# Kernel optimization log

Measured on AMD Instinct MI355X. Metric: run time of the kernel, lower is better.

Reference implementation:

```python
import jax, jax.numpy as jnp
import numpy as np

B, N, C, H = 1, 4096, 512, 8
S = 64  # sqrt(N), static


def setup_inputs() -> dict:
    key = jax.random.key(0)
    ks = jax.random.split(key, 4)
    d = C // H
    return {
        "x": jax.random.normal(ks[0], (B, N, C), dtype=jnp.float32),
        "num_heads": H,
        "bias": jnp.zeros((1,), dtype=jnp.float32),  # unused in original forward
        "scale": jnp.asarray(d ** -0.5, dtype=jnp.float32),
        "Wqkv": jax.random.normal(ks[1], (3 * C, C), dtype=jnp.float32) * (C ** -0.5),
        "bqkv": jnp.zeros((3 * C,), dtype=jnp.float32),
        "Wproj": jax.random.normal(ks[2], (C, C), dtype=jnp.float32) * (C ** -0.5),
        "bproj": jnp.zeros((C,), dtype=jnp.float32),
    }


def reference(x, num_heads, bias, scale, Wqkv, bqkv, Wproj, bproj):
    b, n, c = x.shape
    d = c // num_heads
    # fused QKV projection: [b, n, 3c] -> [3, b, h, n, d]
    qkv = (x @ Wqkv.T + bqkv).reshape(b, n, 3, num_heads, d).transpose(2, 0, 3, 1, 4)
    q, k, v = qkv[0] * scale, qkv[1], qkv[2]
    attn = jax.nn.softmax(jnp.einsum("bhnd,bhmd->bhnm", q, k), axis=-1)
    out = jnp.einsum("bhnm,bhmd->bhnd", attn, v)
    out = out.transpose(0, 2, 1, 3).reshape(b, n, c)
    out = out @ Wproj.T + bproj
    return out.reshape(b, S, S, c)
```

## Files before the change

kernel.cpp:

```cpp
#include <hip/hip_runtime.h>
#include <stdint.h>

#define NTOK 4096
#define CDIM 512
#define HEADS 8
#define DHEAD 64
#define PHEAD (NTOK * DHEAD)

typedef __bf16 bf16x8 __attribute__((ext_vector_type(8)));
typedef float f32x4 __attribute__((ext_vector_type(4)));

__device__ __forceinline__ unsigned short bfbits(float f) {
    return __builtin_bit_cast(unsigned short, (__bf16)f);
}

__device__ __forceinline__ f32x4 mfma32(bf16x8 a, bf16x8 b, f32x4 c) {
    return __builtin_amdgcn_mfma_f32_16x16x32_bf16(a, b, c, 0, 0, 0);
}

__device__ __forceinline__ void async16(unsigned short* lds, const unsigned short* g) {
    __builtin_amdgcn_global_load_lds(
        (const __attribute__((address_space(1))) unsigned int*)g,
        (__attribute__((address_space(3))) unsigned int*)lds, 16, 0, 0);
}

__device__ __forceinline__ void stage8(unsigned short* dst, const float* src) {
    const float4 v0 = *(const float4*)src;
    const float4 v1 = *(const float4*)(src + 4);
    ushort4 o0, o1;
    o0.x = bfbits(v0.x); o0.y = bfbits(v0.y); o0.z = bfbits(v0.z); o0.w = bfbits(v0.w);
    o1.x = bfbits(v1.x); o1.y = bfbits(v1.y); o1.z = bfbits(v1.z); o1.w = bfbits(v1.w);
    *(ushort4*)dst = o0;
    *(ushort4*)(dst + 4) = o1;
}

__global__ __launch_bounds__(256) void gemm_qkv(
    const float* __restrict__ A,
    const float* __restrict__ Bm,
    const float* __restrict__ bias,
    const float* __restrict__ scale_p,
    unsigned short* __restrict__ qkv_out)
{
    const int K = CDIM, Nn = 3 * CDIM; (void)Nn;
    __shared__ __align__(16) unsigned short smem[128 * 136];
    unsigned short* lA = smem;
    unsigned short* lB = smem + 4096;

    const int tid = threadIdx.x;
    const int mBase = blockIdx.y * 128, nBase = blockIdx.x * 128;
    const int lane = tid & 63;
    const int w = __builtin_amdgcn_readfirstlane(tid >> 6);
    const int l16 = lane & 15, quad = lane >> 4;
    const int wr = (w >> 1) * 64, wc = (w & 1) * 64;
    const int srow = tid >> 2, scol = (tid & 3) * 8;

    f32x4 acc[4][4] = {};

    for (int kt = 0; kt < K; kt += 32) {
        __syncthreads();
#pragma unroll
        for (int p = 0; p < 2; ++p) {
            const int r = p * 64 + srow;
            stage8(&lA[r * 32 + scol], &A[(size_t)(mBase + r) * K + kt + scol]);
            stage8(&lB[r * 32 + scol], &Bm[(size_t)(nBase + r) * K + kt + scol]);
        }
        __syncthreads();

        bf16x8 af[4], bfr[4];
#pragma unroll
        for (int i = 0; i < 4; ++i)
            af[i] = *(const bf16x8*)&lA[(wr + i * 16 + l16) * 32 + quad * 8];
#pragma unroll
        for (int j = 0; j < 4; ++j)
            bfr[j] = *(const bf16x8*)&lB[(wc + j * 16 + l16) * 32 + quad * 8];
#pragma unroll
        for (int i = 0; i < 4; ++i)
#pragma unroll
            for (int j = 0; j < 4; ++j)
                acc[i][j] = mfma32(af[i], bfr[j], acc[i][j]);
    }

    const int three = nBase >> 9;
    const float scl = scale_p[0] * 1.44269504f;
    const float mul = (three == 0) ? scl : 1.0f;

    __syncthreads();
#pragma unroll
    for (int i = 0; i < 4; ++i)
#pragma unroll
        for (int j = 0; j < 4; ++j)
#pragma unroll
            for (int r = 0; r < 4; ++r) {
                const int rl = wr + i * 16 + quad * 4 + r;
                const int cl = wc + j * 16 + l16;
                const float v = (acc[i][j][r] + bias[nBase + cl]) * mul;
                smem[rl * 136 + cl] = bfbits(v);
            }
    __syncthreads();

    const size_t base3 = (size_t)three * (PHEAD * HEADS);
    if (three < 2) {
#pragma unroll
        for (int pass = 0; pass < 8; ++pass) {
            const int idx = pass * 256 + tid;
            const int rl16 = idx & 15, qc = (idx >> 4) & 7;
            const int hsel = (idx >> 7) & 1, t16l = (idx >> 8) & 7;
            const uint4 d = *(const uint4*)&smem[(t16l * 16 + rl16) * 136 + hsel * 64 + qc * 8];
            const int hh = ((nBase >> 6) + hsel) & 7;
            const int t16 = (mBase >> 4) + t16l;
            const size_t dst = base3 + (size_t)hh * PHEAD +
                (size_t)(((t16 * 2 + (qc >> 2)) * 64 + (qc & 3) * 16 + rl16) * 8);
            *(uint4*)&qkv_out[dst] = d;
        }
    } else {
#pragma unroll
        for (int pass = 0; pass < 8; ++pass) {
            const int idx = pass * 256 + tid;
            const int l16t = idx & 15, quadt = (idx >> 4) & 3;
            const int dt = (idx >> 6) & 3, k32l = (idx >> 8) & 3, hsel = (idx >> 10) & 1;
            const int col = hsel * 64 + dt * 16 + l16t;
            unsigned short o8[8];
#pragma unroll
            for (int e = 0; e < 4; ++e) {
                o8[e]     = smem[(k32l * 32 + quadt * 4 + e) * 136 + col];
                o8[e + 4] = smem[(k32l * 32 + 16 + quadt * 4 + e) * 136 + col];
            }
            const int hh = ((nBase >> 6) + hsel) & 7;
            const int k32 = (mBase >> 5) + k32l;
            const size_t dst = base3 + (size_t)hh * PHEAD +
                (size_t)(((k32 * 4 + dt) * 64 + quadt * 16 + l16t) * 8);
            *(uint4*)&qkv_out[dst] = *(uint4*)o8;
        }
    }
}

__global__ __launch_bounds__(256) void gemm_proj(
    const unsigned short* __restrict__ A,
    const float* __restrict__ Bm,
    const float* __restrict__ bias,
    float* __restrict__ c_out)
{
    const int K = CDIM, Nn = CDIM;
    __shared__ __align__(16) unsigned short smem[128 * 64];
    unsigned short* lA = smem;
    unsigned short* lB = smem + 4096;

    const int tid = threadIdx.x;
    const int mBase = blockIdx.y * 128, nBase = blockIdx.x * 128;
    const int lane = tid & 63;
    const int w = __builtin_amdgcn_readfirstlane(tid >> 6);
    const int l16 = lane & 15, quad = lane >> 4;
    const int wr = (w >> 1) * 64, wc = (w & 1) * 64;
    const int arow = lane >> 2, acol = (lane & 3) * 8;
    const int srow = tid >> 2, scol = (tid & 3) * 8;

    f32x4 acc[4][4] = {};

    for (int kt = 0; kt < K; kt += 32) {
        __syncthreads();
#pragma unroll
        for (int i = 0; i < 2; ++i) {
            const int r0 = (w * 2 + i) * 16;
            async16(&lA[r0 * 32], &A[(size_t)(mBase + r0 + arow) * K + kt + acol]);
        }
#pragma unroll
        for (int p = 0; p < 2; ++p) {
            const int r = p * 64 + srow;
            stage8(&lB[r * 32 + scol], &Bm[(size_t)(nBase + r) * K + kt + scol]);
        }
        __syncthreads();

        bf16x8 af[4], bfr[4];
#pragma unroll
        for (int i = 0; i < 4; ++i)
            af[i] = *(const bf16x8*)&lA[(wr + i * 16 + l16) * 32 + quad * 8];
#pragma unroll
        for (int j = 0; j < 4; ++j)
            bfr[j] = *(const bf16x8*)&lB[(wc + j * 16 + l16) * 32 + quad * 8];
#pragma unroll
        for (int i = 0; i < 4; ++i)
#pragma unroll
            for (int j = 0; j < 4; ++j)
                acc[i][j] = mfma32(af[i], bfr[j], acc[i][j]);
    }

#pragma unroll
    for (int i = 0; i < 4; ++i)
#pragma unroll
        for (int j = 0; j < 4; ++j)
#pragma unroll
            for (int r = 0; r < 4; ++r) {
                const int grow = mBase + wr + i * 16 + quad * 4 + r;
                const int gcol = nBase + wc + j * 16 + l16;
                c_out[(size_t)grow * Nn + gcol] = acc[i][j][r] + bias[gcol];
            }
}

__global__ __launch_bounds__(256, 4) void flash6_k(
    const unsigned short* __restrict__ qf,
    const unsigned short* __restrict__ kf,
    const unsigned short* __restrict__ vf,
    unsigned short* __restrict__ attn_out)
{
    __shared__ float ldsO[4][32][68];
    __shared__ float sml[4][32];

    const int tid = threadIdx.x;
    const int lane = tid & 63;
    const int w = __builtin_amdgcn_readfirstlane(tid >> 6);
    const int l16 = lane & 15, quad = lane >> 4;
    const int h = blockIdx.x, qb = blockIdx.y;

    const unsigned short* qh = qf + (size_t)h * PHEAD;
    const unsigned short* kb = kf + (size_t)h * PHEAD + w * 65536;
    const unsigned short* vb = vf + (size_t)h * PHEAD + w * 65536;

    bf16x8 qfr[2][2];
#pragma unroll
    for (int qt = 0; qt < 2; ++qt)
#pragma unroll
        for (int ks = 0; ks < 2; ++ks)
            qfr[qt][ks] = *(const bf16x8*)&qh[((qb * 2 + qt) * 2 + ks) * 512 + lane * 8];

    bf16x8 ones;
#pragma unroll
    for (int j = 0; j < 8; ++j) ones[j] = (__bf16)1.0f;

    f32x4 oacc[4][2] = {};
    f32x4 lacc[2] = {};

    bf16x8 kA[4], kB[4];
#pragma unroll
    for (int i = 0; i < 4; ++i)
        kA[i] = *(const bf16x8*)&kb[i * 512 + lane * 8];

    auto body = [&](int g, bf16x8* kuse, bf16x8* kload) {
#pragma unroll
        for (int i = 0; i < 4; ++i)
            kload[i] = *(const bf16x8*)&kb[(g + 1) * 2048 + i * 512 + lane * 8];
        bf16x8 vc[4];
#pragma unroll
        for (int i = 0; i < 4; ++i)
            vc[i] = *(const bf16x8*)&vb[g * 2048 + i * 512 + lane * 8];

        f32x4 s[2][2];
#pragma unroll
        for (int kt = 0; kt < 2; ++kt)
#pragma unroll
            for (int qt = 0; qt < 2; ++qt) {
                f32x4 a = {};
                a = mfma32(kuse[kt * 2 + 0], qfr[qt][0], a);
                a = mfma32(kuse[kt * 2 + 1], qfr[qt][1], a);
                s[kt][qt] = a;
            }

        bf16x8 pf[2];
#pragma unroll
        for (int qt = 0; qt < 2; ++qt) {
            bf16x8 pb;
#pragma unroll
            for (int kt = 0; kt < 2; ++kt)
#pragma unroll
                for (int r = 0; r < 4; ++r)
                    pb[kt * 4 + r] = (__bf16)__builtin_amdgcn_exp2f(s[kt][qt][r]);
            pf[qt] = pb;
            lacc[qt] = mfma32(ones, pb, lacc[qt]);
        }
#pragma unroll
        for (int dt = 0; dt < 4; ++dt)
#pragma unroll
            for (int qt = 0; qt < 2; ++qt)
                oacc[dt][qt] = mfma32(vc[dt], pf[qt], oacc[dt][qt]);
    };

    for (int it = 0; it < 16; ++it) {
        body(it * 2 + 0, kA, kB);
        body(it * 2 + 1, kB, kA);
    }

    if (quad == 0) {
#pragma unroll
        for (int qt = 0; qt < 2; ++qt) sml[w][qt * 16 + l16] = lacc[qt][0];
    }
    __syncthreads();
#pragma unroll
    for (int qt = 0; qt < 2; ++qt) {
        const int q = qt * 16 + l16;
#pragma unroll
        for (int dt = 0; dt < 4; ++dt)
            *(f32x4*)&ldsO[w][q][dt * 16 + quad * 4] = oacc[dt][qt];
    }
    __syncthreads();
    {
        const int q = tid >> 3, dseg = (tid & 7) * 8;
        const float L = sml[0][q] + sml[1][q] + sml[2][q] + sml[3][q];
        const float inv = 1.f / L;
        unsigned short o8[8];
#pragma unroll
        for (int i = 0; i < 8; ++i) {
            const float v = ldsO[0][q][dseg + i] + ldsO[1][q][dseg + i] +
                            ldsO[2][q][dseg + i] + ldsO[3][q][dseg + i];
            o8[i] = bfbits(v * inv);
        }
        *(uint4*)&attn_out[(size_t)(qb * 32 + q) * CDIM + h * DHEAD + dseg] = *(uint4*)o8;
    }
}

extern "C" void kernel_launch(void* const* d_in, const int* in_sizes, int n_in,
                              void* d_out, int out_size, void* d_ws, size_t ws_size,
                              hipStream_t stream) {
    const float* x       = (const float*)d_in[0];
    const float* scale_p = (const float*)d_in[3];
    const float* Wqkv    = (const float*)d_in[4];
    const float* bqkv    = (const float*)d_in[5];
    const float* Wproj   = (const float*)d_in[6];
    const float* bproj   = (const float*)d_in[7];
    float* out = (float*)d_out;

    char* ws = (char*)d_ws;
    const size_t OFF_QKV  = 0;
    const size_t OFF_ATTN = 12582912;
    const size_t NEEDED   = OFF_ATTN + 4194304;
    if (ws_size < NEEDED) return;

    unsigned short* qkvb  = (unsigned short*)(ws + OFF_QKV);
    unsigned short* attnb = (unsigned short*)(ws + OFF_ATTN);

    gemm_qkv<<<dim3(12, 32), 256, 0, stream>>>(x, Wqkv, bqkv, scale_p, qkvb);

    const unsigned short* qfr = qkvb;
    const unsigned short* kfr = qkvb + (size_t)PHEAD * HEADS;
    const unsigned short* vfr = qkvb + (size_t)2 * PHEAD * HEADS;
    flash6_k<<<dim3(8, 128), 256, 0, stream>>>(qfr, kfr, vfr, attnb);

    gemm_proj<<<dim3(4, 32), 256, 0, stream>>>(attnb, Wproj, bproj, out);
}
```

Before: 152.1 us.

## Split attention over key halves with atomic accumulation and deferred normalization

```diff
diff --git a/kernel.cpp b/kernel.cpp
--- a/kernel.cpp
+++ b/kernel.cpp
@@ -16,12 +16,6 @@
 
 __device__ __forceinline__ f32x4 mfma32(bf16x8 a, bf16x8 b, f32x4 c) {
     return __builtin_amdgcn_mfma_f32_16x16x32_bf16(a, b, c, 0, 0, 0);
-}
-
-__device__ __forceinline__ void async16(unsigned short* lds, const unsigned short* g) {
-    __builtin_amdgcn_global_load_lds(
-        (const __attribute__((address_space(1))) unsigned int*)g,
-        (__attribute__((address_space(3))) unsigned int*)lds, 16, 0, 0);
 }
 
 __device__ __forceinline__ void stage8(unsigned short* dst, const float* src) {
@@ -41,7 +35,7 @@
     const float* __restrict__ scale_p,
     unsigned short* __restrict__ qkv_out)
 {
-    const int K = CDIM, Nn = 3 * CDIM; (void)Nn;
+    const int K = CDIM;
     __shared__ __align__(16) unsigned short smem[128 * 136];
     unsigned short* lA = smem;
     unsigned short* lB = smem + 4096;
@@ -134,8 +128,126 @@
     }
 }
 
+__global__ __launch_bounds__(256, 2) void flash7_k(
+    const unsigned short* __restrict__ qf,
+    const unsigned short* __restrict__ kf,
+    const unsigned short* __restrict__ vf,
+    float* __restrict__ attn_acc,
+    float* __restrict__ l_acc)
+{
+    __shared__ float ldsO[2][64][68];
+
+    const int tid = threadIdx.x;
+    const int lane = tid & 63;
+    const int w = __builtin_amdgcn_readfirstlane(tid >> 6);
+    const int l16 = lane & 15, quad = lane >> 4;
+    const int h = blockIdx.x, qb = blockIdx.y, ks = blockIdx.z;
+
+    const unsigned short* qh = qf + (size_t)h * PHEAD;
+    const unsigned short* kb = kf + (size_t)h * PHEAD + ks * 131072 + w * 32768;
+    const unsigned short* vb = vf + (size_t)h * PHEAD + ks * 131072 + w * 32768;
+
+    bf16x8 qfr[4][2];
+#pragma unroll
+    for (int qt = 0; qt < 4; ++qt)
+#pragma unroll
+        for (int d2 = 0; d2 < 2; ++d2)
+            qfr[qt][d2] = *(const bf16x8*)&qh[((qb * 4 + qt) * 2 + d2) * 512 + lane * 8];
+
+    bf16x8 ones;
+#pragma unroll
+    for (int j = 0; j < 8; ++j) ones[j] = (__bf16)1.0f;
+
+    f32x4 oacc[4][4] = {};
+    f32x4 lacc[4] = {};
+
+    bf16x8 kA[4], kB[4];
+#pragma unroll
+    for (int i = 0; i < 4; ++i)
+        kA[i] = *(const bf16x8*)&kb[i * 512 + lane * 8];
+
+    auto body = [&](int g, bf16x8* kuse, bf16x8* kload) {
+#pragma unroll
+        for (int i = 0; i < 4; ++i)
+            kload[i] = *(const bf16x8*)&kb[(g + 1) * 2048 + i * 512 + lane * 8];
+        bf16x8 vc[4];
+#pragma unroll
+        for (int i = 0; i < 4; ++i)
+            vc[i] = *(const bf16x8*)&vb[g * 2048 + i * 512 + lane * 8];
+
+        f32x4 s[2][4];
+#pragma unroll
+        for (int kt = 0; kt < 2; ++kt)
+#pragma unroll
+            for (int qt = 0; qt < 4; ++qt) {
+                f32x4 a = {};
+                a = mfma32(kuse[kt * 2 + 0], qfr[qt][0], a);
+                a = mfma32(kuse[kt * 2 + 1], qfr[qt][1], a);
+                s[kt][qt] = a;
+            }
+
+        bf16x8 pf[4];
+#pragma unroll
+        for (int qt = 0; qt < 4; ++qt) {
+            bf16x8 pb;
+#pragma unroll
+            for (int kt = 0; kt < 2; ++kt)
+#pragma unroll
+                for (int r = 0; r < 4; ++r)
+                    pb[kt * 4 + r] = (__bf16)__builtin_amdgcn_exp2f(s[kt][qt][r]);
+            pf[qt] = pb;
+            lacc[qt] = mfma32(ones, pb, lacc[qt]);
+        }
+#pragma unroll
+        for (int dt = 0; dt < 4; ++dt)
+#pragma unroll
+            for (int qt = 0; qt < 4; ++qt)
+                oacc[dt][qt] = mfma32(vc[dt], pf[qt], oacc[dt][qt]);
+    };
+
+    for (int it = 0; it < 8; ++it) {
+        body(it * 2 + 0, kA, kB);
+        body(it * 2 + 1, kB, kA);
+    }
+
+    if (w == 0 || w == 2) {
+        const int b = w >> 1;
+#pragma unroll
+        for (int qt = 0; qt < 4; ++qt)
+#pragma unroll
+            for (int dt = 0; dt < 4; ++dt)
+                *(f32x4*)&ldsO[b][qt * 16 + l16][dt * 16 + quad * 4] = oacc[dt][qt];
+    }
+    if (quad == 0) {
+#pragma unroll
+        for (int qt = 0; qt < 4; ++qt)
+            atomicAdd(&l_acc[h * NTOK + qb * 64 + qt * 16 + l16], lacc[qt][0]);
+    }
+    __syncthreads();
+    if (w == 1 || w == 3) {
+        const int b = w >> 1;
+#pragma unroll
+        for (int qt = 0; qt < 4; ++qt)
+#pragma unroll
+            for (int dt = 0; dt < 4; ++dt) {
+                float* p = &ldsO[b][qt * 16 + l16][dt * 16 + quad * 4];
+                const f32x4 prev = *(const f32x4*)p;
+                *(f32x4*)p = prev + oacc[dt][qt];
+            }
+    }
+    __syncthreads();
+    {
+        const int q = tid >> 2, db = (tid & 3) * 16;
+        float* dst = &attn_acc[(size_t)(qb * 64 + q) * CDIM + h * DHEAD + db];
+#pragma unroll
+        for (int j = 0; j < 16; ++j)
+            atomicAdd(dst + j, ldsO[0][q][db + j] + ldsO[1][q][db + j]);
+    }
+}
+
 __global__ __launch_bounds__(256) void gemm_proj(
-    const unsigned short* __restrict__ A,
+    const float* __restrict__ A,
+    const float* __restrict__ l_acc,
     const float* __restrict__ Bm,
     const float* __restrict__ bias,
     float* __restrict__ c_out)
@@ -151,21 +263,26 @@
     const int w = __builtin_amdgcn_readfirstlane(tid >> 6);
     const int l16 = lane & 15, quad = lane >> 4;
     const int wr = (w >> 1) * 64, wc = (w & 1) * 64;
-    const int arow = lane >> 2, acol = (lane & 3) * 8;
     const int srow = tid >> 2, scol = (tid & 3) * 8;
 
     f32x4 acc[4][4] = {};
 
     for (int kt = 0; kt < K; kt += 32) {
+        const int head = kt >> 6;
         __syncthreads();
-#pragma unroll
-        for (int i = 0; i < 2; ++i) {
-            const int r0 = (w * 2 + i) * 16;
-            async16(&lA[r0 * 32], &A[(size_t)(mBase + r0 + arow) * K + kt + acol]);
-        }
 #pragma unroll
         for (int p = 0; p < 2; ++p) {
             const int r = p * 64 + srow;
+            const float invl = __builtin_amdgcn_rcpf(l_acc[head * NTOK + mBase + r]);
+            const float4 v0 = *(const float4*)&A[(size_t)(mBase + r) * K + kt + scol];
+            const float4 v1 = *(const float4*)&A[(size_t)(mBase + r) * K + kt + scol + 4];
+            ushort4 o0, o1;
+            o0.x = bfbits(v0.x * invl); o0.y = bfbits(v0.y * invl);
+            o0.z = bfbits(v0.z * invl); o0.w = bfbits(v0.w * invl);
+            o1.x = bfbits(v1.x * invl); o1.y = bfbits(v1.y * invl);
+            o1.z = bfbits(v1.z * invl); o1.w = bfbits(v1.w * invl);
+            *(ushort4*)&lA[r * 32 + scol] = o0;
+            *(ushort4*)&lA[r * 32 + scol + 4] = o1;
             stage8(&lB[r * 32 + scol], &Bm[(size_t)(nBase + r) * K + kt + scol]);
         }
         __syncthreads();
@@ -194,116 +311,6 @@
                 const int gcol = nBase + wc + j * 16 + l16;
                 c_out[(size_t)grow * Nn + gcol] = acc[i][j][r] + bias[gcol];
             }
-}
-
-__global__ __launch_bounds__(256, 4) void flash6_k(
-    const unsigned short* __restrict__ qf,
-    const unsigned short* __restrict__ kf,
-    const unsigned short* __restrict__ vf,
-    unsigned short* __restrict__ attn_out)
-{
-    __shared__ float ldsO[4][32][68];
-    __shared__ float sml[4][32];
-
-    const int tid = threadIdx.x;
-    const int lane = tid & 63;
-    const int w = __builtin_amdgcn_readfirstlane(tid >> 6);
-    const int l16 = lane & 15, quad = lane >> 4;
-    const int h = blockIdx.x, qb = blockIdx.y;
-
-    const unsigned short* qh = qf + (size_t)h * PHEAD;
-    const unsigned short* kb = kf + (size_t)h * PHEAD + w * 65536;
-    const unsigned short* vb = vf + (size_t)h * PHEAD + w * 65536;
-
-    bf16x8 qfr[2][2];
-#pragma unroll
-    for (int qt = 0; qt < 2; ++qt)
-#pragma unroll
-        for (int ks = 0; ks < 2; ++ks)
-            qfr[qt][ks] = *(const bf16x8*)&qh[((qb * 2 + qt) * 2 + ks) * 512 + lane * 8];
-
-    bf16x8 ones;
-#pragma unroll
-    for (int j = 0; j < 8; ++j) ones[j] = (__bf16)1.0f;
-
-    f32x4 oacc[4][2] = {};
-    f32x4 lacc[2] = {};
-
-    bf16x8 kA[4], kB[4];
-#pragma unroll
-    for (int i = 0; i < 4; ++i)
-        kA[i] = *(const bf16x8*)&kb[i * 512 + lane * 8];
-
-    auto body = [&](int g, bf16x8* kuse, bf16x8* kload) {
-#pragma unroll
-        for (int i = 0; i < 4; ++i)
-            kload[i] = *(const bf16x8*)&kb[(g + 1) * 2048 + i * 512 + lane * 8];
-        bf16x8 vc[4];
-#pragma unroll
-        for (int i = 0; i < 4; ++i)
-            vc[i] = *(const bf16x8*)&vb[g * 2048 + i * 512 + lane * 8];
-
-        f32x4 s[2][2];
-#pragma unroll
-        for (int kt = 0; kt < 2; ++kt)
-#pragma unroll
-            for (int qt = 0; qt < 2; ++qt) {
-                f32x4 a = {};
-                a = mfma32(kuse[kt * 2 + 0], qfr[qt][0], a);
-                a = mfma32(kuse[kt * 2 + 1], qfr[qt][1], a);
-                s[kt][qt] = a;
-            }
-
-        bf16x8 pf[2];
-#pragma unroll
-        for (int qt = 0; qt < 2; ++qt) {
-            bf16x8 pb;
-#pragma unroll
-            for (int kt = 0; kt < 2; ++kt)
-#pragma unroll
-                for (int r = 0; r < 4; ++r)
-                    pb[kt * 4 + r] = (__bf16)__builtin_amdgcn_exp2f(s[kt][qt][r]);
-            pf[qt] = pb;
-            lacc[qt] = mfma32(ones, pb, lacc[qt]);
-        }
-#pragma unroll
-        for (int dt = 0; dt < 4; ++dt)
-#pragma unroll
-            for (int qt = 0; qt < 2; ++qt)
-                oacc[dt][qt] = mfma32(vc[dt], pf[qt], oacc[dt][qt]);
-    };
-
-    for (int it = 0; it < 16; ++it) {
-        body(it * 2 + 0, kA, kB);
-        body(it * 2 + 1, kB, kA);
-    }
-
-    if (quad == 0) {
-#pragma unroll
-        for (int qt = 0; qt < 2; ++qt) sml[w][qt * 16 + l16] = lacc[qt][0];
-    }
-    __syncthreads();
-#pragma unroll
-    for (int qt = 0; qt < 2; ++qt) {
-        const int q = qt * 16 + l16;
-#pragma unroll
-        for (int dt = 0; dt < 4; ++dt)
-            *(f32x4*)&ldsO[w][q][dt * 16 + quad * 4] = oacc[dt][qt];
-    }
-    __syncthreads();
-    {
-        const int q = tid >> 3, dseg = (tid & 7) * 8;
-        const float L = sml[0][q] + sml[1][q] + sml[2][q] + sml[3][q];
-        const float inv = 1.f / L;
-        unsigned short o8[8];
-#pragma unroll
-        for (int i = 0; i < 8; ++i) {
-            const float v = ldsO[0][q][dseg + i] + ldsO[1][q][dseg + i] +
-                            ldsO[2][q][dseg + i] + ldsO[3][q][dseg + i];
-            o8[i] = bfbits(v * inv);
-        }
-        *(uint4*)&attn_out[(size_t)(qb * 32 + q) * CDIM + h * DHEAD + dseg] = *(uint4*)o8;
-    }
 }
 
 extern "C" void kernel_launch(void* const* d_in, const int* in_sizes, int n_in,
@@ -320,18 +327,22 @@
     char* ws = (char*)d_ws;
     const size_t OFF_QKV  = 0;
     const size_t OFF_ATTN = 12582912;
-    const size_t NEEDED   = OFF_ATTN + 4194304;
+    const size_t OFF_L    = OFF_ATTN + 8388608;
+    const size_t NEEDED   = OFF_L + 131072;
     if (ws_size < NEEDED) return;
 
-    unsigned short* qkvb  = (unsigned short*)(ws + OFF_QKV);
-    unsigned short* attnb = (unsigned short*)(ws + OFF_ATTN);
+    unsigned short* qkvb = (unsigned short*)(ws + OFF_QKV);
+    float* attn_acc = (float*)(ws + OFF_ATTN);
+    float* l_acc    = (float*)(ws + OFF_L);
+
+    hipMemsetAsync(attn_acc, 0, 8388608 + 131072, stream);
 
     gemm_qkv<<<dim3(12, 32), 256, 0, stream>>>(x, Wqkv, bqkv, scale_p, qkvb);
 
     const unsigned short* qfr = qkvb;
     const unsigned short* kfr = qkvb + (size_t)PHEAD * HEADS;
     const unsigned short* vfr = qkvb + (size_t)2 * PHEAD * HEADS;
-    flash6_k<<<dim3(8, 128), 256, 0, stream>>>(qfr, kfr, vfr, attnb);
-
-    gemm_proj<<<dim3(4, 32), 256, 0, stream>>>(attnb, Wproj, bproj, out);
-}
+    flash7_k<<<dim3(8, 64, 2), 256, 0, stream>>>(qfr, kfr, vfr, attn_acc, l_acc);
+
+    gemm_proj<<<dim3(4, 32), 256, 0, stream>>>(attn_acc, l_acc, Wproj, bproj, out);
+}
```

After: 341.4 us. +124.5%, slower.
